# Kernel optimization log

Hardware: AMD Instinct MI355X
Metric: run time of the kernel (lower is better)

The kernel has to match this reference:

```python
import jax, jax.numpy as jnp
import numpy as np

NB = 16          # n_bits_per_neuron for all three layers
MAX_ITERS = 4    # recurrent state-feedback iterations


def _addresses(bits, conn):
    # bits: [B, T] int32 in {0,1}; conn: [N, NB] int32 indices into T
    g = bits[:, conn]                                   # [B, N, NB]
    w = (jnp.int32(1) << jnp.arange(NB, dtype=jnp.int32))  # LSB-first weights
    return jnp.sum(g * w, axis=-1)                      # [B, N] int32 addresses


def _lookup(table, conn, bits):
    # table: [N, 2^NB] float RAM contents; returns gathered values [B, N]
    addr = _addresses(bits, conn)
    n = table.shape[0]
    return table[jnp.arange(n)[None, :], addr]


def setup_inputs() -> dict:
    key = jax.random.key(0)
    ks = jax.random.split(key, 7)
    B, IN_BITS = 256, 1024
    N_IN, N_ST, N_OUT = 2048, 1024, 512
    TBL = 1 << NB
    x = jax.random.randint(ks[0], (B, IN_BITS), 0, 2, dtype=jnp.int32)
    conn_in = jax.random.randint(ks[1], (N_IN, NB), 0, IN_BITS, dtype=jnp.int32)
    conn_state = jax.random.randint(ks[2], (N_ST, NB), 0, N_IN + N_ST, dtype=jnp.int32)
    conn_out = jax.random.randint(ks[3], (N_OUT, NB), 0, N_IN + N_ST, dtype=jnp.int32)
    mem_in = jax.random.uniform(ks[4], (N_IN, TBL), dtype=jnp.float32)
    mem_state = jax.random.uniform(ks[5], (N_ST, TBL), dtype=jnp.float32)
    mem_out = jax.random.uniform(ks[6], (N_OUT, TBL), dtype=jnp.float32)
    return {"x": x, "conn_in": conn_in, "conn_state": conn_state,
            "conn_out": conn_out, "mem_in": mem_in, "mem_state": mem_state,
            "mem_out": mem_out}


def reference(x, conn_in, conn_state, conn_out, mem_in, mem_state, mem_out):
    # Input layer: bit-address encode raw bits, RAM gather, binarize.
    B = x.shape[0]
    n_state = mem_state.shape[0]
    in_vals = _lookup(mem_in, conn_in, x)               # [B, N_in]
    in_bits = (in_vals > 0.5).astype(jnp.int32)
    # Multi-step recurrence: state layer sees [input_out, prev_state],
    # output layer sees [input_out, current_state].
    state_bits = jnp.zeros((B, n_state), jnp.int32)
    out_vals = jnp.zeros((B, mem_out.shape[0]), mem_out.dtype)
    for _ in range(MAX_ITERS):  # fixed, small unrolled recurrence
        s_in = jnp.concatenate([in_bits, state_bits], axis=1)
        s_vals = _lookup(mem_state, conn_state, s_in)
        state_bits = (s_vals > 0.5).astype(jnp.int32)
        o_in = jnp.concatenate([in_bits, state_bits], axis=1)
        out_vals = _lookup(mem_out, conn_out, o_in)     # [B, N_out]
    return out_vals
```

## Files before the change

### kernel.cpp

```cpp
#include <hip/hip_runtime.h>
#include <stdint.h>

#define NB        16
#define IN_BITS   1024
#define N_IN      2048
#define N_ST      1024
#define N_OUT     512
#define TBL       65536
#define MAX_ITERS 4

__device__ __forceinline__ int gather_addr(const uint8_t* sb, const int* __restrict__ c) {
    const int4* c4 = (const int4*)c;
    int4 a = c4[0], b = c4[1], cc = c4[2], d = c4[3];
    int addr = 0;
    addr |= (int)sb[a.x]  << 0;
    addr |= (int)sb[a.y]  << 1;
    addr |= (int)sb[a.z]  << 2;
    addr |= (int)sb[a.w]  << 3;
    addr |= (int)sb[b.x]  << 4;
    addr |= (int)sb[b.y]  << 5;
    addr |= (int)sb[b.z]  << 6;
    addr |= (int)sb[b.w]  << 7;
    addr |= (int)sb[cc.x] << 8;
    addr |= (int)sb[cc.y] << 9;
    addr |= (int)sb[cc.z] << 10;
    addr |= (int)sb[cc.w] << 11;
    addr |= (int)sb[d.x]  << 12;
    addr |= (int)sb[d.y]  << 13;
    addr |= (int)sb[d.z]  << 14;
    addr |= (int)sb[d.w]  << 15;
    return addr;
}

__global__ __launch_bounds__(1024)
void ram_multistep_kernel(const int*   __restrict__ x,
                          const int*   __restrict__ conn_in,
                          const int*   __restrict__ conn_state,
                          const int*   __restrict__ conn_out,
                          const float* __restrict__ mem_in,
                          const float* __restrict__ mem_state,
                          const float* __restrict__ mem_out,
                          float*       __restrict__ out)
{
    __shared__ uint8_t xb[IN_BITS];
    __shared__ uint8_t bits[N_IN + N_ST];

    const int b   = blockIdx.x;
    const int tid = threadIdx.x;

    if (tid < IN_BITS) xb[tid] = (uint8_t)x[b * IN_BITS + tid];
    if (tid < N_ST)    bits[N_IN + tid] = 0;
    __syncthreads();

    #pragma unroll
    for (int n = tid; n < N_IN; n += 1024) {
        int addr = gather_addr(xb, conn_in + n * NB);
        float v  = mem_in[(size_t)n * TBL + (size_t)addr];
        bits[n]  = (v > 0.5f) ? 1 : 0;
    }
    __syncthreads();

    for (int it = 0; it < MAX_ITERS; ++it) {
        uint8_t nbit = 0;
        if (tid < N_ST) {
            int addr = gather_addr(bits, conn_state + tid * NB);
            float v  = mem_state[(size_t)tid * TBL + (size_t)addr];
            nbit     = (v > 0.5f) ? 1 : 0;
        }
        __syncthreads();
        if (tid < N_ST) bits[N_IN + tid] = nbit;
        __syncthreads();
    }

    if (tid < N_OUT) {
        int addr = gather_addr(bits, conn_out + tid * NB);
        out[b * N_OUT + tid] = mem_out[(size_t)tid * TBL + (size_t)addr];
    }
}

extern "C" void kernel_launch(void* const* d_in, const int* in_sizes, int n_in,
                              void* d_out, int out_size, void* d_ws, size_t ws_size,
                              hipStream_t stream) {
    const int*   x          = (const int*)  d_in[0];
    const int*   conn_in    = (const int*)  d_in[1];
    const int*   conn_state = (const int*)  d_in[2];
    const int*   conn_out   = (const int*)  d_in[3];
    const float* mem_in     = (const float*)d_in[4];
    const float* mem_state  = (const float*)d_in[5];
    const float* mem_out    = (const float*)d_in[6];
    float*       out        = (float*)d_out;

    const int B = in_sizes[0] / IN_BITS;

    hipLaunchKernelGGL(ram_multistep_kernel, dim3(B), dim3(1024), 0, stream,
                       x, conn_in, conn_state, conn_out,
                       mem_in, mem_state, mem_out, out);
}
```

Baseline: 763.6 us.

## Pre-binarize RAM tables into packed bitmaps before the recurrent lookup kernel

Adds a pre-pass that streams the float input-layer and state-layer tables once and packs each `v > 0.5` comparison into 32-bit words in the workspace. The main kernel then gathers single bits from these compact bitmaps instead of doing random float loads from the large tables. The intent is to replace scattered, cache-unfriendly accesses into hundreds of MB with one coalesced sequential pass plus gathers into a ~24 MB bitmap that can stay cache-resident. The cost is a full read of both tables on every call. The new path runs only when the workspace is large enough; otherwise it falls back to the original kernel.

```diff
diff --git a/kernel.cpp b/kernel.cpp
--- a/kernel.cpp
+++ b/kernel.cpp
@@ -7,7 +7,26 @@
 #define N_ST      1024
 #define N_OUT     512
 #define TBL       65536
+#define TBL_W     (TBL / 32)
 #define MAX_ITERS 4
+
+__global__ __launch_bounds__(256)
+void binarize_kernel(const float4* __restrict__ src, uint32_t* __restrict__ dst) {
+    const long t    = (long)blockIdx.x * blockDim.x + threadIdx.x;
+    const int  lane = threadIdx.x & 63;
+
+    float4 v = src[t];
+    uint32_t p = (v.x > 0.5f ? 1u : 0u) | (v.y > 0.5f ? 2u : 0u) |
+                 (v.z > 0.5f ? 4u : 0u) | (v.w > 0.5f ? 8u : 0u);
+    p |= __shfl_xor(p, 1, 64) << 4;
+    p |= __shfl_xor(p, 2, 64) << 8;
+    p |= __shfl_xor(p, 4, 64) << 16;
+
+    if ((lane & 7) == 0) {
+        long word = (t - lane) / 8 + (lane >> 3);
+        dst[word] = p;
+    }
+}
 
 __device__ __forceinline__ int gather_addr(const uint8_t* sb, const int* __restrict__ c) {
     const int4* c4 = (const int4*)c;
@@ -32,15 +51,24 @@
     return addr;
 }
 
+__device__ __forceinline__ uint8_t bit_lookup(const uint32_t* __restrict__ tbl,
+                                              int neuron, int addr) {
+    uint32_t w = tbl[(size_t)neuron * TBL_W + (addr >> 5)];
+    return (uint8_t)((w >> (addr & 31)) & 1u);
+}
+
+template <bool USE_BITS>
 __global__ __launch_bounds__(1024)
-void ram_multistep_kernel(const int*   __restrict__ x,
-                          const int*   __restrict__ conn_in,
-                          const int*   __restrict__ conn_state,
-                          const int*   __restrict__ conn_out,
-                          const float* __restrict__ mem_in,
-                          const float* __restrict__ mem_state,
-                          const float* __restrict__ mem_out,
-                          float*       __restrict__ out)
+void ram_multistep_kernel(const int*      __restrict__ x,
+                          const int*      __restrict__ conn_in,
+                          const int*      __restrict__ conn_state,
+                          const int*      __restrict__ conn_out,
+                          const float*    __restrict__ mem_in,
+                          const float*    __restrict__ mem_state,
+                          const float*    __restrict__ mem_out,
+                          const uint32_t* __restrict__ inbits,
+                          const uint32_t* __restrict__ stbits,
+                          float*          __restrict__ out)
 {
     __shared__ uint8_t xb[IN_BITS];
     __shared__ uint8_t bits[N_IN + N_ST];
@@ -55,8 +83,13 @@
     #pragma unroll
     for (int n = tid; n < N_IN; n += 1024) {
         int addr = gather_addr(xb, conn_in + n * NB);
-        float v  = mem_in[(size_t)n * TBL + (size_t)addr];
-        bits[n]  = (v > 0.5f) ? 1 : 0;
+        uint8_t bit;
+        if (USE_BITS) {
+            bit = bit_lookup(inbits, n, addr);
+        } else {
+            bit = (mem_in[(size_t)n * TBL + (size_t)addr] > 0.5f) ? 1 : 0;
+        }
+        bits[n] = bit;
     }
     __syncthreads();
 
@@ -64,8 +97,11 @@
         uint8_t nbit = 0;
         if (tid < N_ST) {
             int addr = gather_addr(bits, conn_state + tid * NB);
-            float v  = mem_state[(size_t)tid * TBL + (size_t)addr];
-            nbit     = (v > 0.5f) ? 1 : 0;
+            if (USE_BITS) {
+                nbit = bit_lookup(stbits, tid, addr);
+            } else {
+                nbit = (mem_state[(size_t)tid * TBL + (size_t)addr] > 0.5f) ? 1 : 0;
+            }
         }
         __syncthreads();
         if (tid < N_ST) bits[N_IN + tid] = nbit;
@@ -92,7 +128,26 @@
 
     const int B = in_sizes[0] / IN_BITS;
 
-    hipLaunchKernelGGL(ram_multistep_kernel, dim3(B), dim3(1024), 0, stream,
-                       x, conn_in, conn_state, conn_out,
-                       mem_in, mem_state, mem_out, out);
+    const size_t in_words = (size_t)N_IN * TBL_W;
+    const size_t st_words = (size_t)N_ST * TBL_W;
+    const size_t need     = (in_words + st_words) * sizeof(uint32_t);
+
+    if (ws_size >= need) {
+        uint32_t* inbits = (uint32_t*)d_ws;
+        uint32_t* stbits = inbits + in_words;
+
+        hipLaunchKernelGGL(binarize_kernel, dim3((N_IN * (TBL / 4)) / 256), dim3(256),
+                           0, stream, (const float4*)mem_in, inbits);
+        hipLaunchKernelGGL(binarize_kernel, dim3((N_ST * (TBL / 4)) / 256), dim3(256),
+                           0, stream, (const float4*)mem_state, stbits);
+
+        hipLaunchKernelGGL(ram_multistep_kernel<true>, dim3(B), dim3(1024), 0, stream,
+                           x, conn_in, conn_state, conn_out,
+                           mem_in, mem_state, mem_out, inbits, stbits, out);
+    } else {
+        hipLaunchKernelGGL(ram_multistep_kernel<false>, dim3(B), dim3(1024), 0, stream,
+                           x, conn_in, conn_state, conn_out,
+                           mem_in, mem_state, mem_out,
+                           (const uint32_t*)nullptr, (const uint32_t*)nullptr, out);
+    }
 }
```

Measured after the change: 886.2 us. 16.0% more time.
